# Kernel optimization log

Measured on AMD Instinct MI355X. Metric: run time of the kernel, lower is better.

Reference implementation:

```python
import jax, jax.numpy as jnp
import numpy as np

jax.config.update("jax_enable_x64", True)  # original upcasts to double for cdist

B, D, T = 16, 256, 2048
K = 1024  # num_embeddings
COMMITMENT_COST = 0.25


def setup_inputs() -> dict:
    key = jax.random.key(0)
    k1, k2 = jax.random.split(key)
    inputs = jax.random.normal(k1, (B, D, T), dtype=jnp.float32)
    embeddings = jax.random.uniform(k2, (K, D), minval=-1.0 / K, maxval=1.0 / K, dtype=jnp.float32)
    return {"inputs": inputs, "embeddings": embeddings}


def reference(inputs, embeddings):
    b, d, t = inputs.shape
    # [B, D, T] -> [B*T, D]
    flat = jnp.transpose(inputs, (0, 2, 1)).reshape(-1, d)
    # fp64 pairwise squared distances (argmin identical to cdist p=2)
    x = flat.astype(jnp.float64)
    e = embeddings.astype(jnp.float64)
    d2 = (jnp.sum(x * x, axis=1, keepdims=True)
          - 2.0 * (x @ e.T)
          + jnp.sum(e * e, axis=1))  # [N, K]
    encoding_indices = jnp.argmin(d2, axis=1)  # [N]
    quantized = embeddings[encoding_indices].reshape(b, t, d).transpose(0, 2, 1)  # [B, D, T]
    q_detached = jax.lax.stop_gradient(quantized)
    e_latent_loss = jnp.mean((q_detached - inputs) ** 2)
    q_latent_loss = jnp.mean((quantized - jax.lax.stop_gradient(inputs)) ** 2)
    loss = q_latent_loss + COMMITMENT_COST * e_latent_loss
    # straight-through estimator
    quantized_st = inputs + jax.lax.stop_gradient(quantized - inputs)
    return quantized_st, loss, e_latent_loss, q_latent_loss, encoding_indices
```

## Files before the change

### kernel.cpp

```cpp
#include <hip/hip_runtime.h>
#include <hip/hip_bf16.h>

#define NB 16
#define ND 256
#define NT 2048
#define NK 1024
#define NN (NB * NT)
#define QSIZE (NB * ND * NT)
#define SCL_OFF QSIZE
#define IDX_OFF (QSIZE + 3)
#define TAU 4.0e-5f

#define WS_CNT   0
#define WS_PART  64
#define WS_E2F   8448
#define WS_E2D   12544
#define WS_LIST  20736
#define WS_B1S   151808
#define WS_B2S   413952
#define WS_I1S   676096
#define WS_BPACK 938240
#define WS_ET    1986816
#define WS_NEED_ET (WS_ET + 1048576)

typedef __attribute__((ext_vector_type(8))) short bf16x8;
typedef __attribute__((ext_vector_type(4))) float f32x4;
#define MFMA16(a, b, c) __builtin_amdgcn_mfma_f32_16x16x32_bf16(a, b, c, 0, 0, 0)

__device__ inline void bf16split(float v, short& hi, short& lo) {
    union { __hip_bfloat16 b; short s; } uh, ul;
    uh.b = __float2bfloat16(v);
    float hf = __bfloat162float(uh.b);
    ul.b = __float2bfloat16(v - hf);
    hi = uh.s; lo = ul.s;
}

__global__ __launch_bounds__(64) void vq_e2(const float4* __restrict__ E4,
                                            double* __restrict__ e2d,
                                            float* __restrict__ e2f,
                                            float* __restrict__ ET, int use_et,
                                            int* __restrict__ cnt) {
    int k = blockIdx.x;
    int lane = threadIdx.x;
    float4 v = E4[k * 64 + lane];
    if (use_et) {
        ET[(size_t)(4 * lane + 0) * NK + k] = v.x;
        ET[(size_t)(4 * lane + 1) * NK + k] = v.y;
        ET[(size_t)(4 * lane + 2) * NK + k] = v.z;
        ET[(size_t)(4 * lane + 3) * NK + k] = v.w;
    }
    double s = (double)v.x * v.x + (double)v.y * v.y + (double)v.z * v.z + (double)v.w * v.w;
    #pragma unroll
    for (int off = 32; off; off >>= 1) s += __shfl_down(s, off, 64);
    if (lane == 0) { e2d[k] = s; e2f[k] = (float)s; }
    if (k == 0 && lane == 0) cnt[0] = 0;
}

__global__ __launch_bounds__(64) void vq_prep_bpack(const float4* __restrict__ E4,
                                                    uint4* __restrict__ Bp4) {
    const int cc = blockIdx.x >> 3;
    const int ds = blockIdx.x & 7;
    const int lane = threadIdx.x;
    const int c = cc * 16 + (lane & 15);
    const int q = lane >> 4;
    float4 v0 = E4[(size_t)c * 64 + ds * 8 + q * 2];
    float4 v1 = E4[(size_t)c * 64 + ds * 8 + q * 2 + 1];
    float vals[8] = {v0.x, v0.y, v0.z, v0.w, v1.x, v1.y, v1.z, v1.w};
    union { short s[8]; uint4 v; } hi, lo;
    #pragma unroll
    for (int j = 0; j < 8; ++j) bf16split(vals[j], hi.s[j], lo.s[j]);
    Bp4[(size_t)cc * 1024 + ds * 64 + lane]       = hi.v;
    Bp4[(size_t)cc * 1024 + 512 + ds * 64 + lane] = lo.v;
}

__global__ __launch_bounds__(256, 2) void vq_pass1(const float* __restrict__ X,
                                                   const uint4* __restrict__ Bp4,
                                                   const float* __restrict__ e2f,
                                                   float* __restrict__ b1s,
                                                   float* __restrict__ b2s,
                                                   int* __restrict__ i1s) {
    __shared__ uint4 Bl4[2][1024];
    const int tid   = threadIdx.x;
    const int lane  = tid & 63;
    const int w     = tid >> 6;
    const int slice = blockIdx.x & 1;
    const int n0    = (blockIdx.x >> 1) * 128;
    const int b     = n0 >> 11;
    const int t0    = n0 & (NT - 1);
    const int m16   = lane & 15;
    const int q     = lane >> 4;
    const uint4* Bps = Bp4 + (size_t)slice * 32768;

    bf16x8 ah[2][8], al[2][8];
    const float* Xb = X + (size_t)b * (ND * NT);
    #pragma unroll
    for (int t = 0; t < 2; ++t) {
        const int trow = t0 + w * 32 + t * 16 + m16;
        #pragma unroll
        for (int ds = 0; ds < 8; ++ds) {
            #pragma unroll
            for (int j = 0; j < 8; ++j) {
                const int d = ds * 32 + q * 8 + j;
                float v = Xb[(size_t)d * NT + trow];
                short h, l; bf16split(v, h, l);
                ah[t][ds][j] = h; al[t][ds][j] = l;
            }
        }
    }

    float b1[2][4], b2[2][4]; int i1[2][4];
    #pragma unroll
    for (int t = 0; t < 2; ++t)
        #pragma unroll
        for (int r = 0; r < 4; ++r) { b1[t][r] = 3e38f; b2[t][r] = 3e38f; i1[t][r] = 0; }

    uint4 pre[4];
    #pragma unroll
    for (int i = 0; i < 4; ++i) pre[i] = Bps[tid + 256 * i];
    #pragma unroll
    for (int i = 0; i < 4; ++i) Bl4[0][tid + 256 * i] = pre[i];
    __syncthreads();

    for (int cc = 0; cc < 32; ++cc) {
        const bf16x8* Bf = (const bf16x8*)Bl4[cc & 1];
        if (cc < 31) {
            #pragma unroll
            for (int i = 0; i < 4; ++i) pre[i] = Bps[(size_t)(cc + 1) * 1024 + tid + 256 * i];
        }
        f32x4 hh0 = {0.f,0.f,0.f,0.f}, lh0 = {0.f,0.f,0.f,0.f}, hl0 = {0.f,0.f,0.f,0.f};
        f32x4 hh1 = {0.f,0.f,0.f,0.f}, lh1 = {0.f,0.f,0.f,0.f}, hl1 = {0.f,0.f,0.f,0.f};
        #pragma unroll
        for (int ds = 0; ds < 8; ++ds) {
            bf16x8 bh = Bf[ds * 64 + lane];
            bf16x8 bl = Bf[512 + ds * 64 + lane];
            hh0 = MFMA16(ah[0][ds], bh, hh0);
            hh1 = MFMA16(ah[1][ds], bh, hh1);
            lh0 = MFMA16(al[0][ds], bh, lh0);
            lh1 = MFMA16(al[1][ds], bh, lh1);
            hl0 = MFMA16(ah[0][ds], bl, hl0);
            hl1 = MFMA16(ah[1][ds], bl, hl1);
        }
        if (cc < 31) {
            #pragma unroll
            for (int i = 0; i < 4; ++i) Bl4[(cc + 1) & 1][tid + 256 * i] = pre[i];
            __syncthreads();
        }
        const int  code = slice * 512 + cc * 16 + m16;
        const float e2v = e2f[code];
        #pragma unroll
        for (int r = 0; r < 4; ++r) {
            float s0 = e2v - 2.0f * (hh0[r] + lh0[r] + hl0[r]);
            if (s0 < b1[0][r]) { b2[0][r] = b1[0][r]; b1[0][r] = s0; i1[0][r] = code; }
            else if (s0 < b2[0][r]) b2[0][r] = s0;
            float s1 = e2v - 2.0f * (hh1[r] + lh1[r] + hl1[r]);
            if (s1 < b1[1][r]) { b2[1][r] = b1[1][r]; b1[1][r] = s1; i1[1][r] = code; }
            else if (s1 < b2[1][r]) b2[1][r] = s1;
        }
    }

    #pragma unroll
    for (int t = 0; t < 2; ++t) {
        #pragma unroll
        for (int r = 0; r < 4; ++r) {
            float B1 = b1[t][r], B2 = b2[t][r]; int I1 = i1[t][r];
            #pragma unroll
            for (int mm = 1; mm < 16; mm <<= 1) {
                float o1 = __shfl_xor(B1, mm, 16);
                float o2 = __shfl_xor(B2, mm, 16);
                int   oi = __shfl_xor(I1, mm, 16);
                if (o1 < B1 || (o1 == B1 && oi < I1)) { B2 = fminf(B1, o2); B1 = o1; I1 = oi; }
                else B2 = fminf(B2, o1);
            }
            if (m16 == 0) {
                int n = n0 + w * 32 + t * 16 + q * 4 + r;
                int s = slice * NN + n;
                b1s[s] = B1; b2s[s] = B2; i1s[s] = I1;
            }
        }
    }
}

__global__ __launch_bounds__(256) void vq_merge(const float* __restrict__ b1s,
                                                const float* __restrict__ b2s,
                                                const int* __restrict__ i1s,
                                                int* __restrict__ cnt,
                                                int* __restrict__ list,
                                                float* __restrict__ out) {
    const int n = blockIdx.x * 256 + threadIdx.x;
    float a1 = b1s[n],      a2 = b2s[n];      int ai = i1s[n];
    float c1 = b1s[NN + n], c2 = b2s[NN + n]; int ci = i1s[NN + n];
    float B1, B2; int I1;
    if (c1 < a1) { B1 = c1; I1 = ci; B2 = fminf(a1, c2); }
    else         { B1 = a1; I1 = ai; B2 = fminf(a2, c1); }
    out[IDX_OFF + n] = (float)I1;
    if (B2 - B1 < TAU) { int p = atomicAdd(cnt, 1); list[p] = n; }
}

__global__ __launch_bounds__(256, 2) void vq_refine(const float* __restrict__ X,
                                                    const float4* __restrict__ E4,
                                                    const float* __restrict__ ET, int use_et,
                                                    const double* __restrict__ e2d,
                                                    const int* __restrict__ cnt,
                                                    const int* __restrict__ list,
                                                    float* __restrict__ out) {
    __shared__ double xs[4][256];
    __shared__ double sm_s[4][4];
    __shared__ int    sm_k[4][4];
    const int m = cnt[0];
    const int tid = threadIdx.x;
    for (int p = blockIdx.x; p * 4 < m; p += 512) {
        int nrow[4];
        #pragma unroll
        for (int g = 0; g < 4; ++g) {
            int j = p * 4 + g;
            nrow[g] = list[j < m ? j : m - 1];
        }
        #pragma unroll
        for (int g = 0; g < 4; ++g) {
            int n = nrow[g]; int bb = n >> 11; int tt = n & (NT - 1);
            xs[g][tid] = (double)X[((size_t)bb * ND + tid) * NT + tt];
        }
        __syncthreads();
        double acc[4][4];
        #pragma unroll
        for (int kk = 0; kk < 4; ++kk)
            #pragma unroll
            for (int g = 0; g < 4; ++g) acc[kk][g] = 0.0;
        if (use_et) {
            #pragma unroll 2
            for (int dd = 0; dd < 256; ++dd) {
                float e0 = ET[(size_t)dd * NK +   0 + tid];
                float e1 = ET[(size_t)dd * NK + 256 + tid];
                float e2 = ET[(size_t)dd * NK + 512 + tid];
                float e3 = ET[(size_t)dd * NK + 768 + tid];
                #pragma unroll
                for (int g = 0; g < 4; ++g) {
                    double xv = xs[g][dd];
                    acc[0][g] += xv * (double)e0;
                    acc[1][g] += xv * (double)e1;
                    acc[2][g] += xv * (double)e2;
                    acc[3][g] += xv * (double)e3;
                }
            }
        } else {
            for (int dq = 0; dq < 64; ++dq) {
                #pragma unroll
                for (int kk = 0; kk < 4; ++kk) {
                    float4 ev = E4[(size_t)(kk * 256 + tid) * 64 + dq];
                    #pragma unroll
                    for (int g = 0; g < 4; ++g)
                        acc[kk][g] += xs[g][dq*4+0] * (double)ev.x + xs[g][dq*4+1] * (double)ev.y
                                    + xs[g][dq*4+2] * (double)ev.z + xs[g][dq*4+3] * (double)ev.w;
                }
            }
        }
        #pragma unroll
        for (int g = 0; g < 4; ++g) {
            double bs = 1e300; int bk = 0x7fffffff;
            #pragma unroll
            for (int kk = 0; kk < 4; ++kk) {
                int k = kk * 256 + tid;
                double s = e2d[k] - 2.0 * acc[kk][g];
                if (s < bs) { bs = s; bk = k; }
            }
            #pragma unroll
            for (int mm = 1; mm < 64; mm <<= 1) {
                double os = __shfl_xor(bs, mm, 64);
                int    ok = __shfl_xor(bk, mm, 64);
                if (os < bs || (os == bs && ok < bk)) { bs = os; bk = ok; }
            }
            if ((tid & 63) == 0) { sm_s[tid >> 6][g] = bs; sm_k[tid >> 6][g] = bk; }
        }
        __syncthreads();
        if (tid < 4) {
            double Bv = 1e300; int Kv = 0x7fffffff;
            for (int ww = 0; ww < 4; ++ww) {
                double s2 = sm_s[ww][tid]; int k2 = sm_k[ww][tid];
                if (s2 < Bv || (s2 == Bv && k2 < Kv)) { Bv = s2; Kv = k2; }
            }
            if (p * 4 + tid < m) out[IDX_OFF + nrow[tid]] = (float)Kv;
        }
        __syncthreads();
    }
}

__global__ __launch_bounds__(256) void vq_gather(const float* __restrict__ X,
                                                 const float4* __restrict__ E4,
                                                 float* __restrict__ out,
                                                 double* __restrict__ part) {
    __shared__ float Eq[32 * 257];
    __shared__ double sm[4];
    const int bt = blockIdx.x;
    const int b  = bt >> 6;
    const int t0 = (bt & 63) << 5;
    const float* irowf = out + IDX_OFF + b * NT + t0;
    {
        const int r  = threadIdx.x >> 3;
        const int l8 = threadIdx.x & 7;
        const int id = (int)irowf[r];
        const float4* er = E4 + (size_t)id * 64;
        #pragma unroll
        for (int it = 0; it < 8; ++it) {
            int c = l8 + (it << 3);
            float4 v = er[c];
            float* p = &Eq[r * 257 + 4 * c];
            p[0] = v.x; p[1] = v.y; p[2] = v.z; p[3] = v.w;
        }
    }
    __syncthreads();
    const int tw = threadIdx.x & 31;
    const int dg = threadIdx.x >> 5;
    double ls = 0.0;
    #pragma unroll 8
    for (int it = 0; it < 32; ++it) {
        const int d = dg + (it << 3);
        const float qv = Eq[tw * 257 + d];
        const size_t off = ((size_t)b * ND + d) * NT + t0 + tw;
        const float x = X[off];
        out[off] = x + (qv - x);
        const double df = (double)qv - (double)x;
        ls = fma(df, df, ls);
    }
    #pragma unroll
    for (int o = 32; o; o >>= 1) ls += __shfl_down(ls, o, 64);
    if ((threadIdx.x & 63) == 0) sm[threadIdx.x >> 6] = ls;
    __syncthreads();
    if (threadIdx.x == 0) part[bt] = sm[0] + sm[1] + sm[2] + sm[3];
}

__global__ __launch_bounds__(256) void vq_final(const double* __restrict__ part,
                                                float* __restrict__ out) {
    __shared__ double sm[4];
    const int tid = threadIdx.x;
    double s = part[tid] + part[tid + 256] + part[tid + 512] + part[tid + 768];
    #pragma unroll
    for (int o = 32; o; o >>= 1) s += __shfl_down(s, o, 64);
    if ((tid & 63) == 0) sm[tid >> 6] = s;
    __syncthreads();
    if (tid == 0) {
        double mse = (sm[0] + sm[1] + sm[2] + sm[3]) * (1.0 / (double)QSIZE);
        out[SCL_OFF + 0] = (float)(1.25 * mse);
        out[SCL_OFF + 1] = (float)mse;
        out[SCL_OFF + 2] = (float)mse;
    }
}

extern "C" void kernel_launch(void* const* d_in, const int* in_sizes, int n_in,
                              void* d_out, int out_size, void* d_ws, size_t ws_size,
                              hipStream_t stream) {
    const float* X = (const float*)d_in[0];
    const float* E = (const float*)d_in[1];
    float* out = (float*)d_out;

    char* ws = (char*)d_ws;
    int*    cnt   = (int*)   (ws + WS_CNT);
    double* part  = (double*)(ws + WS_PART);
    float*  e2f   = (float*) (ws + WS_E2F);
    double* e2d   = (double*)(ws + WS_E2D);
    int*    list  = (int*)   (ws + WS_LIST);
    float*  b1s   = (float*) (ws + WS_B1S);
    float*  b2s   = (float*) (ws + WS_B2S);
    int*    i1s   = (int*)   (ws + WS_I1S);
    uint4*  bpack = (uint4*) (ws + WS_BPACK);
    float*  et    = (float*) (ws + WS_ET);
    const int use_et = (ws_size >= (size_t)WS_NEED_ET) ? 1 : 0;

    vq_e2        <<<NK, 64, 0, stream>>>((const float4*)E, e2d, e2f, et, use_et, cnt);
    vq_prep_bpack<<<512, 64, 0, stream>>>((const float4*)E, bpack);
    vq_pass1     <<<NN / 64, 256, 0, stream>>>(X, bpack, e2f, b1s, b2s, i1s);
    vq_merge     <<<NN / 256, 256, 0, stream>>>(b1s, b2s, i1s, cnt, list, out);
    vq_refine    <<<512, 256, 0, stream>>>(X, (const float4*)E, et, use_et, e2d, cnt, list, out);
    vq_gather    <<<NB * (NT / 32), 256, 0, stream>>>(X, (const float4*)E, out, part);
    vq_final     <<<1, 256, 0, stream>>>(part, out);
}
```

Measured before the change: 216.2 us.

## Split codebook into four slices, fuse prep kernels and merge into refine

Pass1 now splits the codebook across four slices instead of two, doubling grid size and raising occupancy hint to 4 blocks per CU. The two embedding-prep kernels are fused into one, and the separate merge kernel with a global atomic list is folded into refine, which merges slice results per 64-row block and builds its ambiguity list in LDS via ballot. Indices are stored as 16-bit. This removes two launches and the global atomic, but each pass1 block redoes its X load and bf16 split for half the codes, and refine work is now unevenly spread across blocks.

```diff
diff --git a/kernel.cpp b/kernel.cpp
--- a/kernel.cpp
+++ b/kernel.cpp
@@ -10,17 +10,16 @@
 #define SCL_OFF QSIZE
 #define IDX_OFF (QSIZE + 3)
 #define TAU 4.0e-5f
-
-#define WS_CNT   0
-#define WS_PART  64
-#define WS_E2F   8448
-#define WS_E2D   12544
-#define WS_LIST  20736
-#define WS_B1S   151808
-#define WS_B2S   413952
-#define WS_I1S   676096
-#define WS_BPACK 938240
-#define WS_ET    1986816
+#define NSLICE 4
+
+#define WS_PART  0
+#define WS_E2F   8192
+#define WS_E2D   12288
+#define WS_B1S   20480
+#define WS_B2S   544768
+#define WS_I1S   1069056
+#define WS_BPACK 1331200
+#define WS_ET    2379776
 #define WS_NEED_ET (WS_ET + 1048576)
 
 typedef __attribute__((ext_vector_type(8))) short bf16x8;
@@ -35,13 +34,13 @@
     hi = uh.s; lo = ul.s;
 }
 
-__global__ __launch_bounds__(64) void vq_e2(const float4* __restrict__ E4,
-                                            double* __restrict__ e2d,
-                                            float* __restrict__ e2f,
-                                            float* __restrict__ ET, int use_et,
-                                            int* __restrict__ cnt) {
-    int k = blockIdx.x;
-    int lane = threadIdx.x;
+__global__ __launch_bounds__(64) void vq_prep(const float4* __restrict__ E4,
+                                              double* __restrict__ e2d,
+                                              float* __restrict__ e2f,
+                                              float* __restrict__ ET, int use_et,
+                                              uint4* __restrict__ Bp4) {
+    const int k = blockIdx.x;
+    const int lane = threadIdx.x;
     float4 v = E4[k * 64 + lane];
     if (use_et) {
         ET[(size_t)(4 * lane + 0) * NK + k] = v.x;
@@ -49,47 +48,45 @@
         ET[(size_t)(4 * lane + 2) * NK + k] = v.z;
         ET[(size_t)(4 * lane + 3) * NK + k] = v.w;
     }
+    float4 a, b2v;
+    a.x = __shfl(v.x, 2 * lane, 64); a.y = __shfl(v.y, 2 * lane, 64);
+    a.z = __shfl(v.z, 2 * lane, 64); a.w = __shfl(v.w, 2 * lane, 64);
+    b2v.x = __shfl(v.x, 2 * lane + 1, 64); b2v.y = __shfl(v.y, 2 * lane + 1, 64);
+    b2v.z = __shfl(v.z, 2 * lane + 1, 64); b2v.w = __shfl(v.w, 2 * lane + 1, 64);
+    if (lane < 32) {
+        const int ds = lane >> 2, q = lane & 3;
+        const int cc = k >> 4;
+        const int fl = q * 16 + (k & 15);
+        float vals[8] = {a.x, a.y, a.z, a.w, b2v.x, b2v.y, b2v.z, b2v.w};
+        union { short s[8]; uint4 u; } hi, lo;
+        #pragma unroll
+        for (int j = 0; j < 8; ++j) bf16split(vals[j], hi.s[j], lo.s[j]);
+        Bp4[(size_t)cc * 1024 + ds * 64 + fl]       = hi.u;
+        Bp4[(size_t)cc * 1024 + 512 + ds * 64 + fl] = lo.u;
+    }
     double s = (double)v.x * v.x + (double)v.y * v.y + (double)v.z * v.z + (double)v.w * v.w;
     #pragma unroll
     for (int off = 32; off; off >>= 1) s += __shfl_down(s, off, 64);
     if (lane == 0) { e2d[k] = s; e2f[k] = (float)s; }
-    if (k == 0 && lane == 0) cnt[0] = 0;
-}
-
-__global__ __launch_bounds__(64) void vq_prep_bpack(const float4* __restrict__ E4,
-                                                    uint4* __restrict__ Bp4) {
-    const int cc = blockIdx.x >> 3;
-    const int ds = blockIdx.x & 7;
-    const int lane = threadIdx.x;
-    const int c = cc * 16 + (lane & 15);
-    const int q = lane >> 4;
-    float4 v0 = E4[(size_t)c * 64 + ds * 8 + q * 2];
-    float4 v1 = E4[(size_t)c * 64 + ds * 8 + q * 2 + 1];
-    float vals[8] = {v0.x, v0.y, v0.z, v0.w, v1.x, v1.y, v1.z, v1.w};
-    union { short s[8]; uint4 v; } hi, lo;
-    #pragma unroll
-    for (int j = 0; j < 8; ++j) bf16split(vals[j], hi.s[j], lo.s[j]);
-    Bp4[(size_t)cc * 1024 + ds * 64 + lane]       = hi.v;
-    Bp4[(size_t)cc * 1024 + 512 + ds * 64 + lane] = lo.v;
-}
-
-__global__ __launch_bounds__(256, 2) void vq_pass1(const float* __restrict__ X,
+}
+
+__global__ __launch_bounds__(256, 4) void vq_pass1(const float* __restrict__ X,
                                                    const uint4* __restrict__ Bp4,
                                                    const float* __restrict__ e2f,
                                                    float* __restrict__ b1s,
                                                    float* __restrict__ b2s,
-                                                   int* __restrict__ i1s) {
+                                                   unsigned short* __restrict__ i1s) {
     __shared__ uint4 Bl4[2][1024];
     const int tid   = threadIdx.x;
     const int lane  = tid & 63;
     const int w     = tid >> 6;
-    const int slice = blockIdx.x & 1;
-    const int n0    = (blockIdx.x >> 1) * 128;
+    const int slice = blockIdx.x & 3;
+    const int n0    = (blockIdx.x >> 2) * 128;
     const int b     = n0 >> 11;
     const int t0    = n0 & (NT - 1);
     const int m16   = lane & 15;
     const int q     = lane >> 4;
-    const uint4* Bps = Bp4 + (size_t)slice * 32768;
+    const uint4* Bps = Bp4 + (size_t)slice * 16384;
 
     bf16x8 ah[2][8], al[2][8];
     const float* Xb = X + (size_t)b * (ND * NT);
@@ -121,9 +118,9 @@
     for (int i = 0; i < 4; ++i) Bl4[0][tid + 256 * i] = pre[i];
     __syncthreads();
 
-    for (int cc = 0; cc < 32; ++cc) {
+    for (int cc = 0; cc < 16; ++cc) {
         const bf16x8* Bf = (const bf16x8*)Bl4[cc & 1];
-        if (cc < 31) {
+        if (cc < 15) {
             #pragma unroll
             for (int i = 0; i < 4; ++i) pre[i] = Bps[(size_t)(cc + 1) * 1024 + tid + 256 * i];
         }
@@ -140,12 +137,12 @@
             hl0 = MFMA16(ah[0][ds], bl, hl0);
             hl1 = MFMA16(ah[1][ds], bl, hl1);
         }
-        if (cc < 31) {
+        if (cc < 15) {
             #pragma unroll
             for (int i = 0; i < 4; ++i) Bl4[(cc + 1) & 1][tid + 256 * i] = pre[i];
             __syncthreads();
         }
-        const int  code = slice * 512 + cc * 16 + m16;
+        const int  code = slice * 256 + cc * 16 + m16;
         const float e2v = e2f[code];
         #pragma unroll
         for (int r = 0; r < 4; ++r) {
@@ -173,47 +170,55 @@
             }
             if (m16 == 0) {
                 int n = n0 + w * 32 + t * 16 + q * 4 + r;
-                int s = slice * NN + n;
-                b1s[s] = B1; b2s[s] = B2; i1s[s] = I1;
-            }
-        }
-    }
-}
-
-__global__ __launch_bounds__(256) void vq_merge(const float* __restrict__ b1s,
-                                                const float* __restrict__ b2s,
-                                                const int* __restrict__ i1s,
-                                                int* __restrict__ cnt,
-                                                int* __restrict__ list,
-                                                float* __restrict__ out) {
-    const int n = blockIdx.x * 256 + threadIdx.x;
-    float a1 = b1s[n],      a2 = b2s[n];      int ai = i1s[n];
-    float c1 = b1s[NN + n], c2 = b2s[NN + n]; int ci = i1s[NN + n];
-    float B1, B2; int I1;
-    if (c1 < a1) { B1 = c1; I1 = ci; B2 = fminf(a1, c2); }
-    else         { B1 = a1; I1 = ai; B2 = fminf(a2, c1); }
-    out[IDX_OFF + n] = (float)I1;
-    if (B2 - B1 < TAU) { int p = atomicAdd(cnt, 1); list[p] = n; }
+                size_t s = (size_t)slice * NN + n;
+                b1s[s] = B1; b2s[s] = B2; i1s[s] = (unsigned short)I1;
+            }
+        }
+    }
 }
 
 __global__ __launch_bounds__(256, 2) void vq_refine(const float* __restrict__ X,
                                                     const float4* __restrict__ E4,
                                                     const float* __restrict__ ET, int use_et,
                                                     const double* __restrict__ e2d,
-                                                    const int* __restrict__ cnt,
-                                                    const int* __restrict__ list,
+                                                    const float* __restrict__ b1s,
+                                                    const float* __restrict__ b2s,
+                                                    const unsigned short* __restrict__ i1s,
                                                     float* __restrict__ out) {
     __shared__ double xs[4][256];
     __shared__ double sm_s[4][4];
     __shared__ int    sm_k[4][4];
-    const int m = cnt[0];
+    __shared__ int    lds_list[64];
+    __shared__ int    lds_cnt;
     const int tid = threadIdx.x;
-    for (int p = blockIdx.x; p * 4 < m; p += 512) {
+    const int nb0 = blockIdx.x * 64;
+
+    if (tid < 64) {
+        const int n = nb0 + tid;
+        float B1 = b1s[n], B2 = b2s[n]; int I1 = i1s[n];
+        #pragma unroll
+        for (int s = 1; s < NSLICE; ++s) {
+            float c1 = b1s[(size_t)s * NN + n], c2 = b2s[(size_t)s * NN + n];
+            int   ci = i1s[(size_t)s * NN + n];
+            if (c1 < B1) { B2 = fminf(B1, c2); B1 = c1; I1 = ci; }
+            else          B2 = fminf(B2, c1);
+        }
+        out[IDX_OFF + n] = (float)I1;
+        const bool flag = (B2 - B1 < TAU);
+        unsigned long long mask = __ballot(flag);
+        int pos = __popcll(mask & ((1ull << tid) - 1ull));
+        if (flag) lds_list[pos] = n;
+        if (tid == 0) lds_cnt = (int)__popcll(mask);
+    }
+    __syncthreads();
+    const int m = lds_cnt;
+
+    for (int j0 = 0; j0 < m; j0 += 4) {
         int nrow[4];
         #pragma unroll
         for (int g = 0; g < 4; ++g) {
-            int j = p * 4 + g;
-            nrow[g] = list[j < m ? j : m - 1];
+            int j = j0 + g;
+            nrow[g] = lds_list[j < m ? j : m - 1];
         }
         #pragma unroll
         for (int g = 0; g < 4; ++g) {
@@ -278,7 +283,7 @@
                 double s2 = sm_s[ww][tid]; int k2 = sm_k[ww][tid];
                 if (s2 < Bv || (s2 == Bv && k2 < Kv)) { Bv = s2; Kv = k2; }
             }
-            if (p * 4 + tid < m) out[IDX_OFF + nrow[tid]] = (float)Kv;
+            if (j0 + tid < m) out[IDX_OFF + nrow[tid]] = (float)Kv;
         }
         __syncthreads();
     }
@@ -353,23 +358,20 @@
     float* out = (float*)d_out;
 
     char* ws = (char*)d_ws;
-    int*    cnt   = (int*)   (ws + WS_CNT);
     double* part  = (double*)(ws + WS_PART);
     float*  e2f   = (float*) (ws + WS_E2F);
     double* e2d   = (double*)(ws + WS_E2D);
-    int*    list  = (int*)   (ws + WS_LIST);
     float*  b1s   = (float*) (ws + WS_B1S);
     float*  b2s   = (float*) (ws + WS_B2S);
-    int*    i1s   = (int*)   (ws + WS_I1S);
+    unsigned short* i1s = (unsigned short*)(ws + WS_I1S);
     uint4*  bpack = (uint4*) (ws + WS_BPACK);
     float*  et    = (float*) (ws + WS_ET);
     const int use_et = (ws_size >= (size_t)WS_NEED_ET) ? 1 : 0;
 
-    vq_e2        <<<NK, 64, 0, stream>>>((const float4*)E, e2d, e2f, et, use_et, cnt);
-    vq_prep_bpack<<<512, 64, 0, stream>>>((const float4*)E, bpack);
-    vq_pass1     <<<NN / 64, 256, 0, stream>>>(X, bpack, e2f, b1s, b2s, i1s);
-    vq_merge     <<<NN / 256, 256, 0, stream>>>(b1s, b2s, i1s, cnt, list, out);
-    vq_refine    <<<512, 256, 0, stream>>>(X, (const float4*)E, et, use_et, e2d, cnt, list, out);
-    vq_gather    <<<NB * (NT / 32), 256, 0, stream>>>(X, (const float4*)E, out, part);
-    vq_final     <<<1, 256, 0, stream>>>(part, out);
-}
+    vq_prep  <<<NK, 64, 0, stream>>>((const float4*)E, e2d, e2f, et, use_et, bpack);
+    vq_pass1 <<<(NN / 128) * NSLICE, 256, 0, stream>>>(X, bpack, e2f, b1s, b2s, i1s);
+    vq_refine<<<NN / 64, 256, 0, stream>>>(X, (const float4*)E, et, use_et, e2d,
+                                           b1s, b2s, i1s, out);
+    vq_gather<<<NB * (NT / 32), 256, 0, stream>>>(X, (const float4*)E, out, part);
+    vq_final <<<1, 256, 0, stream>>>(part, out);
+}
```

After: 376.1 us. 1.74x slower.
